# Performance work log

Measured on AMD Instinct MI355X. Metric: run time of the kernel, lower is better.

## Reference

```python
import jax, jax.numpy as jnp
import numpy as np
import math

B, N, D, H = 16, 200, 2048, 2048  # batch, seq (== max_len), feature dim, hidden/output dim


def setup_inputs() -> dict:
    key = jax.random.key(0)
    ks = jax.random.split(key, 16)
    s = 1.0 / math.sqrt(D)
    return {
        "input_query": jax.random.normal(ks[0], (B, N, D), jnp.float32),
        "input_key": jax.random.normal(ks[1], (B, N, D), jnp.float32),
        "input_value": jax.random.normal(ks[2], (B, N, D), jnp.float32),
        "loc_vector": jax.random.normal(ks[3], (B, N, D), jnp.float32),
        "Wq": jax.random.normal(ks[4], (D, H), jnp.float32) * s,
        "bq": jnp.zeros((H,), jnp.float32),
        "Wk": jax.random.normal(ks[5], (D, H), jnp.float32) * s,
        "bk": jnp.zeros((H,), jnp.float32),
        "Wv": jax.random.normal(ks[6], (D, H), jnp.float32) * s,
        "bv": jnp.zeros((H,), jnp.float32),
        "Wloc": jax.random.normal(ks[7], (D, H), jnp.float32) * s,
        "bloc": jnp.zeros((H,), jnp.float32),
        "Wlk": jax.random.normal(ks[8], (D, H), jnp.float32) * s,
        "blk": jnp.zeros((H,), jnp.float32),
        "param": jax.random.normal(ks[9], (B, N, H), jnp.float32),
    }


def reference(input_query, input_key, input_value, loc_vector,
              Wq, bq, Wk, bk, Wv, bv, Wloc, bloc, Wlk, blk, param):
    n = input_query.shape[1]
    lq = input_query @ Wq + bq                      # (b, n, h)
    lk = input_key @ Wk + bk                        # (b, m, h)
    lv = input_value @ Wv + bv                      # (b, m, o)
    loc = loc_vector[:, :n, :]
    lloc = loc @ Wloc + bloc                        # (b, n, h)
    kloc = loc @ Wlk + blk                          # (b, n, h)
    p = param[: input_query.shape[0], :n, :]        # (b, n, h)
    # Fused multi-term scores: (Q+P)K^T + (Q+Lloc)Kloc^T  == QK^T + Lloc Kloc^T + P K^T + Q Kloc^T
    scores = (jnp.einsum('bnh,bmh->bnm', lq + p, lk)
              + jnp.einsum('bnh,bmh->bnm', lq + lloc, kloc))
    attn = jax.nn.softmax(scores / math.sqrt(lq.shape[-1]), axis=-1)
    return jnp.einsum('bnm,bmo->bno', attn, lv)     # (b, n, o); dropout is identity in eval
```

## Files before the change

### kernel.cpp

```cpp
#include <hip/hip_runtime.h>
#include <hip/hip_bf16.h>
#include <math.h>

typedef float floatx4 __attribute__((ext_vector_type(4)));
typedef __bf16 bf16x8 __attribute__((ext_vector_type(8)));
typedef unsigned short ushort_t;

__device__ __forceinline__ ushort_t f2bf(float f) {
    union { float f; unsigned int i; } v; v.f = f;
    unsigned int i = v.i;
    return (ushort_t)((i + 0x7FFFu + ((i >> 16) & 1u)) >> 16);
}
__device__ __forceinline__ unsigned int pack2(float a, float b) {
    return (unsigned int)f2bf(a) | ((unsigned int)f2bf(b) << 16);
}
__device__ __forceinline__ floatx4 mfma16(bf16x8 a, bf16x8 b, floatx4 c) {
    return __builtin_amdgcn_mfma_f32_16x16x32_bf16(a, b, c, 0, 0, 0);
}
__device__ __forceinline__ void load_lds16(const ushort_t* g, ushort_t* l) {
    __builtin_amdgcn_global_load_lds(
        (const __attribute__((address_space(1))) unsigned int*)g,
        (__attribute__((address_space(3))) unsigned int*)l, 16, 0, 0);
}

#define G_SB   __builtin_amdgcn_sched_barrier(0)
#define G_BAR  __builtin_amdgcn_s_barrier()
#define WVM8   asm volatile("s_waitcnt vmcnt(8)" ::: "memory")
#define WVM0   asm volatile("s_waitcnt vmcnt(0)" ::: "memory")

__global__ __launch_bounds__(256) void k_convert(const float* __restrict__ q, const float* __restrict__ k,
                          const float* __restrict__ v, const float* __restrict__ loc,
                          ushort_t* qb, ushort_t* kb, ushort_t* vb, ushort_t* locb) {
    int z = blockIdx.y;
    const float* src = z == 0 ? q : z == 1 ? k : z == 2 ? v : loc;
    ushort_t* dst    = z == 0 ? qb : z == 1 ? kb : z == 2 ? vb : locb;
    size_t idx = (size_t)blockIdx.x * 256 + threadIdx.x;
    floatx4 f = *(const floatx4*)(src + idx * 4);
    uint2 o;
    o.x = pack2(f[0], f[1]);
    o.y = pack2(f[2], f[3]);
    *(uint2*)(dst + idx * 4) = o;
}

__global__ void k_wtrans(const float* __restrict__ w0, const float* __restrict__ w1,
                         const float* __restrict__ w2, const float* __restrict__ w3,
                         const float* __restrict__ w4,
                         ushort_t* t0, ushort_t* t1, ushort_t* t2, ushort_t* t3, ushort_t* t4) {
    __shared__ float tile[32][33];
    int z = blockIdx.z;
    const float* W = z == 0 ? w0 : z == 1 ? w1 : z == 2 ? w2 : z == 3 ? w3 : w4;
    ushort_t* T    = z == 0 ? t0 : z == 1 ? t1 : z == 2 ? t2 : z == 3 ? t3 : t4;
    int n0 = blockIdx.x * 32, k0 = blockIdx.y * 32;
    int tx = threadIdx.x & 31, ty = threadIdx.x >> 5;
#pragma unroll
    for (int i = 0; i < 4; i++) {
        int row = ty + i * 8;
        tile[row][tx] = W[(size_t)(k0 + row) * 2048 + n0 + tx];
    }
    __syncthreads();
#pragma unroll
    for (int i = 0; i < 4; i++) {
        int row = ty + i * 8;
        T[(size_t)(n0 + row) * 2048 + k0 + tx] = f2bf(tile[tx][row]);
    }
}

__global__ void k_vtrans(const ushort_t* __restrict__ lv, ushort_t* __restrict__ lvT) {
    __shared__ ushort_t tile[32][33];
    int n0 = blockIdx.x * 32;
    int t0 = blockIdx.y * 32;
    int b = blockIdx.z;
    int tx = threadIdx.x & 31, ty = threadIdx.x >> 5;
#pragma unroll
    for (int i = 0; i < 4; i++) {
        int row = ty + i * 8;
        int tk = t0 + row;
        ushort_t v = 0;
        if (tk < 200) v = lv[(size_t)(b * 200 + tk) * 2048 + n0 + tx];
        tile[row][tx] = v;
    }
    __syncthreads();
#pragma unroll
    for (int i = 0; i < 4; i++) {
        int row = ty + i * 8;
        lvT[((size_t)b * 2048 + n0 + row) * 224 + t0 + tx] = tile[tx][row];
    }
}

__global__ __launch_bounds__(256, 2) void k_gemm(
    const ushort_t* A0, const ushort_t* A1, const ushort_t* A2, const ushort_t* A3, const ushort_t* A4,
    const ushort_t* W0, const ushort_t* W1, const ushort_t* W2, const ushort_t* W3, const ushort_t* W4,
    const float* B0, const float* B1, const float* B2, const float* B3, const float* B4,
    ushort_t* lqp, ushort_t* lvp, ushort_t* llocp, ushort_t* kcat) {
    int bid = blockIdx.x;
    int tileid = (bid & 7) * 250 + (bid >> 3);
    int z = tileid / 400;
    int r = tileid - z * 400;
    int nt = r / 25;
    int mt = r - nt * 25;
    int m0 = mt * 128, n0 = nt * 128;

    const ushort_t* A  = z == 0 ? A0 : z == 1 ? A1 : z == 2 ? A2 : z == 3 ? A3 : A4;
    const ushort_t* Wt = z == 0 ? W0 : z == 1 ? W1 : z == 2 ? W2 : z == 3 ? W3 : W4;
    const float* bias  = z == 0 ? B0 : z == 1 ? B1 : z == 2 ? B2 : z == 3 ? B3 : B4;

    __shared__ ushort_t As[2][128 * 64];
    __shared__ ushort_t Bs[2][128 * 64];

    int tid = threadIdx.x;
    int lane = tid & 63, w = tid >> 6;
    int quad = lane >> 4, col = lane & 15;
    int wr = w >> 1, wc = w & 1;

    int sl = lane >> 3;
    int sc = ((lane & 7) ^ sl) * 8;
    const ushort_t* Ag[4]; const ushort_t* Bg[4]; int ldst[4];
#pragma unroll
    for (int u = 0; u < 4; u++) {
        int rowoff = u * 32 + w * 8;
        Ag[u] = A  + (size_t)(m0 + rowoff + sl) * 2048 + sc;
        Bg[u] = Wt + (size_t)(n0 + rowoff + sl) * 2048 + sc;
        ldst[u] = rowoff * 64;
    }

#define STG(KT, BUF) do { int kk = (KT) * 64;              \
        load_lds16(Ag[0] + kk, As[BUF] + ldst[0]);         \
        load_lds16(Ag[1] + kk, As[BUF] + ldst[1]);         \
        load_lds16(Ag[2] + kk, As[BUF] + ldst[2]);         \
        load_lds16(Ag[3] + kk, As[BUF] + ldst[3]);         \
        load_lds16(Bg[0] + kk, Bs[BUF] + ldst[0]);         \
        load_lds16(Bg[1] + kk, Bs[BUF] + ldst[1]);         \
        load_lds16(Bg[2] + kk, Bs[BUF] + ldst[2]);         \
        load_lds16(Bg[3] + kk, Bs[BUF] + ldst[3]); } while (0)

    int sw = col & 7;
    int ko0 = (quad ^ sw) * 8;
    int ko1 = ((4 | quad) ^ sw) * 8;
    int aro[4], bro[4];
#pragma unroll
    for (int mi = 0; mi < 4; mi++) aro[mi] = (wr * 64 + mi * 16 + col) * 64;
#pragma unroll
    for (int ni = 0; ni < 4; ni++) bro[ni] = (wc * 64 + ni * 16 + col) * 64;

    floatx4 acc[4][4] = {};

#define CMP(BUF) do {                                                     \
        bf16x8 af[4][2], bfr[4][2];                                       \
        _Pragma("unroll") for (int mi = 0; mi < 4; mi++) {                \
            af[mi][0] = *(const bf16x8*)&As[BUF][aro[mi] + ko0];          \
            af[mi][1] = *(const bf16x8*)&As[BUF][aro[mi] + ko1]; }        \
        _Pragma("unroll") for (int ni = 0; ni < 4; ni++) {                \
            bfr[ni][0] = *(const bf16x8*)&Bs[BUF][bro[ni] + ko0];         \
            bfr[ni][1] = *(const bf16x8*)&Bs[BUF][bro[ni] + ko1]; }       \
        __builtin_amdgcn_s_setprio(1);                                    \
        _Pragma("unroll") for (int mi = 0; mi < 4; mi++)                  \
        _Pragma("unroll") for (int ni = 0; ni < 4; ni++) {                \
            acc[mi][ni] = mfma16(af[mi][0], bfr[ni][0], acc[mi][ni]);     \
            acc[mi][ni] = mfma16(af[mi][1], bfr[ni][1], acc[mi][ni]); }   \
        __builtin_amdgcn_s_setprio(0); } while (0)

    STG(0, 0);
#pragma unroll 1
    for (int tt = 0; tt < 16; tt++) {
        int t0k = tt * 2;
        STG(t0k + 1, 1);
        WVM8;
        G_SB; G_BAR; G_SB;
        CMP(0);
        G_SB; G_BAR;
        STG((t0k + 2) & 31, 0);
        WVM8;
        G_SB; G_BAR; G_SB;
        CMP(1);
        G_SB; G_BAR;
    }
    WVM0;

    ushort_t* Cplain = z == 0 ? lqp : z == 2 ? lvp : llocp;
    int kcoff = (z == 4) ? 2048 : 0;
    bool to_kcat = (z == 1 || z == 4);
    float bvv[4];
#pragma unroll
    for (int ni = 0; ni < 4; ni++) bvv[ni] = bias[n0 + wc * 64 + ni * 16 + col];
#pragma unroll
    for (int mi = 0; mi < 4; mi++) {
#pragma unroll
        for (int r2 = 0; r2 < 4; r2++) {
            int m = m0 + wr * 64 + mi * 16 + quad * 4 + r2;
            ushort_t* crow;
            if (to_kcat) {
                int bb = m / 200, rr = m - bb * 200;
                crow = kcat + (size_t)(bb * 224 + rr) * 4096 + kcoff;
            } else {
                crow = Cplain + (size_t)m * 2048;
            }
#pragma unroll
            for (int ni = 0; ni < 4; ni++) {
                int n = n0 + wc * 64 + ni * 16 + col;
                crow[n] = f2bf(acc[mi][ni][r2] + bvv[ni]);
            }
        }
    }
#undef STG
#undef CMP
}

__global__ __launch_bounds__(256) void k_qprep(const ushort_t* __restrict__ lqp,
                                               const ushort_t* __restrict__ llocp,
                                               const float* __restrict__ param,
                                               ushort_t* __restrict__ qcat) {
    int m = blockIdx.x;
    int b = m / 200, r = m - b * 200;
    int c = threadIdx.x * 8;
    bf16x8 ql = *(const bf16x8*)(lqp + (size_t)m * 2048 + c);
    bf16x8 ll = *(const bf16x8*)(llocp + (size_t)m * 2048 + c);
    floatx4 p0 = *(const floatx4*)(param + (size_t)m * 2048 + c);
    floatx4 p1 = *(const floatx4*)(param + (size_t)m * 2048 + c + 4);
    bf16x8 q1, q2;
#pragma unroll
    for (int j = 0; j < 4; j++) {
        q1[j]     = (__bf16)((float)ql[j] + p0[j]);
        q1[j + 4] = (__bf16)((float)ql[j + 4] + p1[j]);
        q2[j]     = (__bf16)((float)ql[j] + (float)ll[j]);
        q2[j + 4] = (__bf16)((float)ql[j + 4] + (float)ll[j + 4]);
    }
    ushort_t* dst = qcat + ((size_t)(b * 224 + r)) * 4096 + c;
    *(bf16x8*)dst = q1;
    *(bf16x8*)(dst + 2048) = q2;
}

__global__ __launch_bounds__(256, 2) void k_scores(const ushort_t* __restrict__ qcat,
                                                   const ushort_t* __restrict__ kcat,
                                                   float* __restrict__ part) {
    int bid = blockIdx.x;
    int tile = (bid & 7) * 56 + (bid >> 3);
    int qt = tile % 7;
    int t2 = tile / 7;
    int b  = t2 & 15;
    int kc = t2 >> 4;

    __shared__ ushort_t S[2][256 * 64];

    int tid = threadIdx.x;
    int lane = tid & 63, w = tid >> 6;
    int quad = lane >> 4, col = lane & 15;

    int sl = lane >> 3;
    int sc = ((lane & 7) ^ sl) * 8;

    const ushort_t* qbase = qcat + ((size_t)b * 224 + qt * 32) * 4096 + kc * 1024;
    const ushort_t* kbase = kcat + (size_t)b * 224 * 4096 + kc * 1024;

    const ushort_t* gsrc[8]; int ldst[8];
#pragma unroll
    for (int u = 0; u < 8; u++) {
        int row = u * 32 + w * 8;
        gsrc[u] = (u == 0) ? qbase + (size_t)(row + sl) * 4096 + sc
                           : kbase + (size_t)(row - 32 + sl) * 4096 + sc;
        ldst[u] = row * 64;
    }

#define SSTG(KT, BUF) do { int kk = (KT) * 64;                        \
        _Pragma("unroll") for (int u = 0; u < 8; u++)                 \
            load_lds16(gsrc[u] + kk, S[BUF] + ldst[u]); } while (0)

    int sw = col & 7;
    int ko0 = (quad ^ sw) * 8;
    int ko1 = ((4 | quad) ^ sw) * 8;

    floatx4 acc[2][4] = {};

#define SCMP(BUF) do {                                                    \
        bf16x8 af[2][2];                                                  \
        _Pragma("unroll") for (int mi = 0; mi < 2; mi++) {                \
            int ar = (mi * 16 + col) * 64;                                \
            af[mi][0] = *(const bf16x8*)&S[BUF][ar + ko0];                \
            af[mi][1] = *(const bf16x8*)&S[BUF][ar + ko1]; }              \
        __builtin_amdgcn_s_setprio(1);                                    \
        _Pragma("unroll") for (int fi = 0; fi < 4; fi++) {                \
            int f = w + fi * 4;                                           \
            if (f < 14) {                                                 \
                int br = (32 + f * 16 + col) * 64;                        \
                bf16x8 b0 = *(const bf16x8*)&S[BUF][br + ko0];            \
                bf16x8 b1 = *(const bf16x8*)&S[BUF][br + ko1];            \
                _Pragma("unroll") for (int mi = 0; mi < 2; mi++) {        \
                    acc[mi][fi] = mfma16(af[mi][0], b0, acc[mi][fi]);     \
                    acc[mi][fi] = mfma16(af[mi][1], b1, acc[mi][fi]); }   \
            } }                                                           \
        __builtin_amdgcn_s_setprio(0); } while (0)

    SSTG(0, 0);
#pragma unroll 1
    for (int tt = 0; tt < 8; tt++) {
        SSTG(2 * tt + 1, 1);
        WVM8; G_SB; G_BAR; G_SB;
        SCMP(0);
        G_SB; G_BAR;
        SSTG((2 * tt + 2) & 15, 0);
        WVM8; G_SB; G_BAR; G_SB;
        SCMP(1);
        G_SB; G_BAR;
    }
    WVM0;

    float* pbase = part + ((size_t)(kc * 16 + b) * 224 + qt * 32) * 224;
#pragma unroll
    for (int fi = 0; fi < 4; fi++) {
        int f = w + fi * 4;
        if (f < 14) {
#pragma unroll
            for (int mi = 0; mi < 2; mi++)
#pragma unroll
                for (int r = 0; r < 4; r++)
                    pbase[(mi * 16 + quad * 4 + r) * 224 + f * 16 + col] = acc[mi][fi][r];
        }
    }
#undef SSTG
#undef SCMP
}

__global__ __launch_bounds__(256) void k_softmax(const float* __restrict__ part,
                                                 ushort_t* __restrict__ attn) {
    int row = blockIdx.x * 8 + (threadIdx.x >> 5);
    int b = row / 200, r = row - b * 200;
    int p = threadIdx.x & 31;
    const float* p0 = part + ((size_t)b * 224 + r) * 224;
    const size_t st = (size_t)16 * 224 * 224;
    const float scale = 0.022097086912079608f;
    float ev[7];
    float mx = -1e30f;
#pragma unroll
    for (int j = 0; j < 7; j++) {
        int c = p * 7 + j;
        float v = (c < 200) ? (p0[c] + p0[c + st] + p0[c + 2 * st] + p0[c + 3 * st]) * scale
                            : -1e30f;
        ev[j] = v;
        mx = fmaxf(mx, v);
    }
#pragma unroll
    for (int m = 1; m < 32; m <<= 1) mx = fmaxf(mx, __shfl_xor(mx, m, 32));
    float s = 0.f;
#pragma unroll
    for (int j = 0; j < 7; j++) {
        float e = __expf(ev[j] - mx);
        ev[j] = e;
        s += e;
    }
#pragma unroll
    for (int m = 1; m < 32; m <<= 1) s += __shfl_xor(s, m, 32);
    float rs = 1.0f / s;
    ushort_t* arow = attn + (size_t)row * 224;
#pragma unroll
    for (int j = 0; j < 7; j++) {
        int c = p * 7 + j;
        arow[c] = (c < 200) ? f2bf(ev[j] * rs) : (ushort_t)0;
    }
}

__global__ __launch_bounds__(256) void k_pv(const ushort_t* __restrict__ attn,
                                            const ushort_t* __restrict__ lvT,
                                            float* __restrict__ out) {
    int nt = blockIdx.x;
    int qt = blockIdx.y;
    int b = blockIdx.z;
    int tid = threadIdx.x, lane = tid & 63, w = tid >> 6;
    int quad = lane >> 4, col = lane & 15;
    const ushort_t* arow[2];
#pragma unroll
    for (int mi = 0; mi < 2; mi++) {
        int aq = qt * 32 + mi * 16 + col; if (aq > 199) aq = 199;
        arow[mi] = attn + (size_t)(b * 200 + aq) * 224;
    }
    int nbase = nt * 256 + w * 64;
    const ushort_t* bp[4];
#pragma unroll
    for (int ni = 0; ni < 4; ni++)
        bp[ni] = lvT + ((size_t)b * 2048 + nbase + ni * 16 + col) * 224;
    floatx4 acc[2][4] = {};
#pragma unroll
    for (int k0 = 0; k0 < 224; k0 += 32) {
        int ko = k0 + quad * 8;
        bf16x8 av[2];
#pragma unroll
        for (int mi = 0; mi < 2; mi++) av[mi] = *(const bf16x8*)(arow[mi] + ko);
#pragma unroll
        for (int ni = 0; ni < 4; ni++) {
            bf16x8 bv = *(const bf16x8*)(bp[ni] + ko);
#pragma unroll
            for (int mi = 0; mi < 2; mi++) acc[mi][ni] = mfma16(av[mi], bv, acc[mi][ni]);
        }
    }
#pragma unroll
    for (int mi = 0; mi < 2; mi++) {
#pragma unroll
        for (int r = 0; r < 4; r++) {
            int m = qt * 32 + mi * 16 + quad * 4 + r;
            if (m < 200) {
#pragma unroll
                for (int ni = 0; ni < 4; ni++) {
                    int n = nbase + ni * 16 + col;
                    out[(size_t)(b * 200 + m) * 2048 + n] = acc[mi][ni][r];
                }
            }
        }
    }
}

extern "C" void kernel_launch(void* const* d_in, const int* in_sizes, int n_in,
                              void* d_out, int out_size, void* d_ws, size_t ws_size,
                              hipStream_t stream) {
    (void)in_sizes; (void)n_in; (void)out_size; (void)ws_size;
    const float* q    = (const float*)d_in[0];
    const float* k    = (const float*)d_in[1];
    const float* v    = (const float*)d_in[2];
    const float* loc  = (const float*)d_in[3];
    const float* Wq   = (const float*)d_in[4];
    const float* bq   = (const float*)d_in[5];
    const float* Wk   = (const float*)d_in[6];
    const float* bk   = (const float*)d_in[7];
    const float* Wv   = (const float*)d_in[8];
    const float* bv   = (const float*)d_in[9];
    const float* Wloc = (const float*)d_in[10];
    const float* bloc = (const float*)d_in[11];
    const float* Wlk  = (const float*)d_in[12];
    const float* blk  = (const float*)d_in[13];
    const float* param = (const float*)d_in[14];
    float* out = (float*)d_out;

    size_t off = 0;
    auto nxt = [&](size_t bytes) {
        void* p = (char*)d_ws + off;
        off += (bytes + 255) & ~(size_t)255;
        return p;
    };
    ushort_t* wt[5];
    for (int i = 0; i < 5; i++) wt[i] = (ushort_t*)nxt(2048ull * 2048 * 2);
    ushort_t* qb    = (ushort_t*)nxt(3200ull * 2048 * 2);
    ushort_t* kb    = (ushort_t*)nxt(3200ull * 2048 * 2);
    ushort_t* vb    = (ushort_t*)nxt(3200ull * 2048 * 2);
    ushort_t* locb  = (ushort_t*)nxt(3200ull * 2048 * 2);
    ushort_t* lqp   = (ushort_t*)nxt(3200ull * 2048 * 2);
    ushort_t* llocp = (ushort_t*)nxt(3200ull * 2048 * 2);
    ushort_t* lvp   = (ushort_t*)nxt(3200ull * 2048 * 2);
    ushort_t* kcat  = (ushort_t*)nxt(16ull * 224 * 4096 * 2);
    ushort_t* lvT  = wt[0];
    ushort_t* attn = wt[0] + 16ull * 2048 * 224;
    float*    part = (float*)(attn + 3200ull * 224);
    ushort_t* qcat = qb;

    k_convert<<<dim3(6400, 4), 256, 0, stream>>>(q, k, v, loc, qb, kb, vb, locb);
    k_wtrans<<<dim3(64, 64, 5), 256, 0, stream>>>(Wq, Wk, Wv, Wloc, Wlk,
                                                  wt[0], wt[1], wt[2], wt[3], wt[4]);
    k_gemm<<<dim3(2000), 256, 0, stream>>>(qb, kb, vb, locb, locb,
                                           wt[0], wt[1], wt[2], wt[3], wt[4],
                                           bq, bk, bv, bloc, blk,
                                           lqp, lvp, llocp, kcat);
    k_qprep<<<dim3(3200), 256, 0, stream>>>(lqp, llocp, param, qcat);
    k_vtrans<<<dim3(64, 7, 16), 256, 0, stream>>>(lvp, lvT);
    k_scores<<<dim3(448), 256, 0, stream>>>(qcat, kcat, part);
    k_softmax<<<dim3(400), 256, 0, stream>>>(part, attn);
    k_pv<<<dim3(8, 7, 16), 256, 0, stream>>>(attn, lvT, out);
}
```

Before: 432.1 us.

## Fuse prep kernels and write V projection transposed from GEMM epilogue

The separate input-conversion and weight-transpose kernels become one k_prep launch with 64x64 weight-transpose tiles. The same launch also zero-fills the padding columns of the transposed V buffer. The V-projection GEMM epilogue now writes its output directly into the transposed lvT layout, so the k_vtrans pass and the intermediate lvp buffer are gone. The per-batch key row stride in kcat shrinks from 224 to 208, which costs strided 2-byte scattered stores in the V epilogue and lets the score kernel's padding-row loads read neighbouring data.

```diff
diff --git a/kernel.cpp b/kernel.cpp
--- a/kernel.cpp
+++ b/kernel.cpp
@@ -28,62 +28,52 @@
 #define WVM8   asm volatile("s_waitcnt vmcnt(8)" ::: "memory")
 #define WVM0   asm volatile("s_waitcnt vmcnt(0)" ::: "memory")
 
-__global__ __launch_bounds__(256) void k_convert(const float* __restrict__ q, const float* __restrict__ k,
-                          const float* __restrict__ v, const float* __restrict__ loc,
-                          ushort_t* qb, ushort_t* kb, ushort_t* vb, ushort_t* locb) {
-    int z = blockIdx.y;
-    const float* src = z == 0 ? q : z == 1 ? k : z == 2 ? v : loc;
-    ushort_t* dst    = z == 0 ? qb : z == 1 ? kb : z == 2 ? vb : locb;
-    size_t idx = (size_t)blockIdx.x * 256 + threadIdx.x;
-    floatx4 f = *(const floatx4*)(src + idx * 4);
-    uint2 o;
-    o.x = pack2(f[0], f[1]);
-    o.y = pack2(f[2], f[3]);
-    *(uint2*)(dst + idx * 4) = o;
-}
-
-__global__ void k_wtrans(const float* __restrict__ w0, const float* __restrict__ w1,
-                         const float* __restrict__ w2, const float* __restrict__ w3,
-                         const float* __restrict__ w4,
-                         ushort_t* t0, ushort_t* t1, ushort_t* t2, ushort_t* t3, ushort_t* t4) {
-    __shared__ float tile[32][33];
-    int z = blockIdx.z;
-    const float* W = z == 0 ? w0 : z == 1 ? w1 : z == 2 ? w2 : z == 3 ? w3 : w4;
-    ushort_t* T    = z == 0 ? t0 : z == 1 ? t1 : z == 2 ? t2 : z == 3 ? t3 : t4;
-    int n0 = blockIdx.x * 32, k0 = blockIdx.y * 32;
-    int tx = threadIdx.x & 31, ty = threadIdx.x >> 5;
-#pragma unroll
-    for (int i = 0; i < 4; i++) {
-        int row = ty + i * 8;
-        tile[row][tx] = W[(size_t)(k0 + row) * 2048 + n0 + tx];
-    }
-    __syncthreads();
-#pragma unroll
-    for (int i = 0; i < 4; i++) {
-        int row = ty + i * 8;
-        T[(size_t)(n0 + row) * 2048 + k0 + tx] = f2bf(tile[tx][row]);
-    }
-}
-
-__global__ void k_vtrans(const ushort_t* __restrict__ lv, ushort_t* __restrict__ lvT) {
-    __shared__ ushort_t tile[32][33];
-    int n0 = blockIdx.x * 32;
-    int t0 = blockIdx.y * 32;
-    int b = blockIdx.z;
-    int tx = threadIdx.x & 31, ty = threadIdx.x >> 5;
-#pragma unroll
-    for (int i = 0; i < 4; i++) {
-        int row = ty + i * 8;
-        int tk = t0 + row;
-        ushort_t v = 0;
-        if (tk < 200) v = lv[(size_t)(b * 200 + tk) * 2048 + n0 + tx];
-        tile[row][tx] = v;
-    }
-    __syncthreads();
-#pragma unroll
-    for (int i = 0; i < 4; i++) {
-        int row = ty + i * 8;
-        lvT[((size_t)b * 2048 + n0 + row) * 224 + t0 + tx] = tile[tx][row];
+__global__ __launch_bounds__(256) void k_prep(
+    const float* __restrict__ q, const float* __restrict__ k,
+    const float* __restrict__ v, const float* __restrict__ loc,
+    const float* __restrict__ w0, const float* __restrict__ w1, const float* __restrict__ w2,
+    const float* __restrict__ w3, const float* __restrict__ w4,
+    ushort_t* qb, ushort_t* kb, ushort_t* vb, ushort_t* locb,
+    ushort_t* t0, ushort_t* t1, ushort_t* t2, ushort_t* t3, ushort_t* t4,
+    ushort_t* lvT) {
+    __shared__ float tile[64][65];
+    int blk = blockIdx.x;
+    if (blk < 12800) {
+        int z = blk / 3200, i = blk - z * 3200;
+        const float* src = z == 0 ? q : z == 1 ? k : z == 2 ? v : loc;
+        ushort_t* dst    = z == 0 ? qb : z == 1 ? kb : z == 2 ? vb : locb;
+        size_t base = ((size_t)i * 256 + threadIdx.x) * 8;
+        floatx4 f0 = *(const floatx4*)(src + base);
+        floatx4 f1 = *(const floatx4*)(src + base + 4);
+        uint4 o;
+        o.x = pack2(f0[0], f0[1]); o.y = pack2(f0[2], f0[3]);
+        o.z = pack2(f1[0], f1[1]); o.w = pack2(f1[2], f1[3]);
+        *(uint4*)(dst + base) = o;
+    } else if (blk < 17920) {
+        int t = blk - 12800;
+        int z = t / 1024, rr = t - z * 1024;
+        const float* W = z == 0 ? w0 : z == 1 ? w1 : z == 2 ? w2 : z == 3 ? w3 : w4;
+        ushort_t* T    = z == 0 ? t0 : z == 1 ? t1 : z == 2 ? t2 : z == 3 ? t3 : t4;
+        int n0 = (rr & 31) * 64, k0 = (rr >> 5) * 64;
+        int tx = threadIdx.x & 63, ty = threadIdx.x >> 6;
+#pragma unroll
+        for (int i = 0; i < 16; i++) {
+            int row = ty + i * 4;
+            tile[row][tx] = W[(size_t)(k0 + row) * 2048 + n0 + tx];
+        }
+        __syncthreads();
+#pragma unroll
+        for (int i = 0; i < 16; i++) {
+            int row = ty + i * 4;
+            T[(size_t)(n0 + row) * 2048 + k0 + tx] = f2bf(tile[tx][row]);
+        }
+    } else {
+        int t = blk - 17920;
+        size_t e = ((size_t)t * 256 + threadIdx.x) * 8;
+        int row = (int)(e / 24);
+        int c = (int)(e - (size_t)row * 24);
+        uint4 zz = {0, 0, 0, 0};
+        *(uint4*)(lvT + (size_t)row * 224 + 200 + c) = zz;
     }
 }
 
@@ -91,7 +81,7 @@
     const ushort_t* A0, const ushort_t* A1, const ushort_t* A2, const ushort_t* A3, const ushort_t* A4,
     const ushort_t* W0, const ushort_t* W1, const ushort_t* W2, const ushort_t* W3, const ushort_t* W4,
     const float* B0, const float* B1, const float* B2, const float* B3, const float* B4,
-    ushort_t* lqp, ushort_t* lvp, ushort_t* llocp, ushort_t* kcat) {
+    ushort_t* lqp, ushort_t* lvT, ushort_t* llocp, ushort_t* kcat) {
     int bid = blockIdx.x;
     int tileid = (bid & 7) * 250 + (bid >> 3);
     int z = tileid / 400;
@@ -176,28 +166,45 @@
     }
     WVM0;
 
-    ushort_t* Cplain = z == 0 ? lqp : z == 2 ? lvp : llocp;
-    int kcoff = (z == 4) ? 2048 : 0;
-    bool to_kcat = (z == 1 || z == 4);
     float bvv[4];
 #pragma unroll
     for (int ni = 0; ni < 4; ni++) bvv[ni] = bias[n0 + wc * 64 + ni * 16 + col];
-#pragma unroll
-    for (int mi = 0; mi < 4; mi++) {
-#pragma unroll
-        for (int r2 = 0; r2 < 4; r2++) {
-            int m = m0 + wr * 64 + mi * 16 + quad * 4 + r2;
-            ushort_t* crow;
-            if (to_kcat) {
+    if (z == 2) {
+#pragma unroll
+        for (int mi = 0; mi < 4; mi++) {
+#pragma unroll
+            for (int r2 = 0; r2 < 4; r2++) {
+                int m = m0 + wr * 64 + mi * 16 + quad * 4 + r2;
                 int bb = m / 200, rr = m - bb * 200;
-                crow = kcat + (size_t)(bb * 224 + rr) * 4096 + kcoff;
-            } else {
-                crow = Cplain + (size_t)m * 2048;
+                ushort_t* cb = lvT + (size_t)bb * 2048 * 224 + rr;
+#pragma unroll
+                for (int ni = 0; ni < 4; ni++) {
+                    int n = n0 + wc * 64 + ni * 16 + col;
+                    cb[(size_t)n * 224] = f2bf(acc[mi][ni][r2] + bvv[ni]);
+                }
             }
-#pragma unroll
-            for (int ni = 0; ni < 4; ni++) {
-                int n = n0 + wc * 64 + ni * 16 + col;
-                crow[n] = f2bf(acc[mi][ni][r2] + bvv[ni]);
+        }
+    } else {
+        ushort_t* Cplain = z == 0 ? lqp : llocp;
+        int kcoff = (z == 4) ? 2048 : 0;
+        bool to_kcat = (z == 1 || z == 4);
+#pragma unroll
+        for (int mi = 0; mi < 4; mi++) {
+#pragma unroll
+            for (int r2 = 0; r2 < 4; r2++) {
+                int m = m0 + wr * 64 + mi * 16 + quad * 4 + r2;
+                ushort_t* crow;
+                if (to_kcat) {
+                    int bb = m / 200, rr = m - bb * 200;
+                    crow = kcat + (size_t)(bb * 208 + rr) * 4096 + kcoff;
+                } else {
+                    crow = Cplain + (size_t)m * 2048;
+                }
+#pragma unroll
+                for (int ni = 0; ni < 4; ni++) {
+                    int n = n0 + wc * 64 + ni * 16 + col;
+                    crow[n] = f2bf(acc[mi][ni][r2] + bvv[ni]);
+                }
             }
         }
     }
@@ -249,7 +256,7 @@
     int sc = ((lane & 7) ^ sl) * 8;
 
     const ushort_t* qbase = qcat + ((size_t)b * 224 + qt * 32) * 4096 + kc * 1024;
-    const ushort_t* kbase = kcat + (size_t)b * 224 * 4096 + kc * 1024;
+    const ushort_t* kbase = kcat + (size_t)b * 208 * 4096 + kc * 1024;
 
     const ushort_t* gsrc[8]; int ldst[8];
 #pragma unroll
@@ -441,22 +448,20 @@
     ushort_t* locb  = (ushort_t*)nxt(3200ull * 2048 * 2);
     ushort_t* lqp   = (ushort_t*)nxt(3200ull * 2048 * 2);
     ushort_t* llocp = (ushort_t*)nxt(3200ull * 2048 * 2);
-    ushort_t* lvp   = (ushort_t*)nxt(3200ull * 2048 * 2);
-    ushort_t* kcat  = (ushort_t*)nxt(16ull * 224 * 4096 * 2);
-    ushort_t* lvT  = wt[0];
-    ushort_t* attn = wt[0] + 16ull * 2048 * 224;
+    ushort_t* kcat  = (ushort_t*)nxt(16ull * 208 * 4096 * 2);
+    ushort_t* lvT   = (ushort_t*)nxt(16ull * 2048 * 224 * 2);
+    ushort_t* attn = wt[0];
     float*    part = (float*)(attn + 3200ull * 224);
     ushort_t* qcat = qb;
 
-    k_convert<<<dim3(6400, 4), 256, 0, stream>>>(q, k, v, loc, qb, kb, vb, locb);
-    k_wtrans<<<dim3(64, 64, 5), 256, 0, stream>>>(Wq, Wk, Wv, Wloc, Wlk,
-                                                  wt[0], wt[1], wt[2], wt[3], wt[4]);
+    k_prep<<<dim3(18304), 256, 0, stream>>>(q, k, v, loc, Wq, Wk, Wv, Wloc, Wlk,
+                                            qb, kb, vb, locb,
+                                            wt[0], wt[1], wt[2], wt[3], wt[4], lvT);
     k_gemm<<<dim3(2000), 256, 0, stream>>>(qb, kb, vb, locb, locb,
                                            wt[0], wt[1], wt[2], wt[3], wt[4],
                                            bq, bk, bv, bloc, blk,
-                                           lqp, lvp, llocp, kcat);
+                                           lqp, lvT, llocp, kcat);
     k_qprep<<<dim3(3200), 256, 0, stream>>>(lqp, llocp, param, qcat);
-    k_vtrans<<<dim3(64, 7, 16), 256, 0, stream>>>(lvp, lvT);
     k_scores<<<dim3(448), 256, 0, stream>>>(qcat, kcat, part);
     k_softmax<<<dim3(400), 256, 0, stream>>>(part, attn);
     k_pv<<<dim3(8, 7, 16), 256, 0, stream>>>(attn, lvT, out);
```

Result: slower. 458.7 us (+6.2%).
